# Kernel optimization log

Hardware: AMD Instinct MI355X
Metric: run time of the kernel (lower is better)

The kernel has to match this reference:

```python
import jax, jax.numpy as jnp
import numpy as np

N_NODES = 1_000_000
N_EDGES = 16_000_000
N_IN, HID, N_OUT = 128, 32, 16


def setup_inputs() -> dict:
    key = jax.random.key(0)
    ks = jax.random.split(key, 8)
    x = jax.random.normal(ks[0], (N_NODES, N_IN), dtype=jnp.float32)
    edge_index = jax.random.randint(ks[1], (2, N_EDGES), 0, N_NODES, dtype=jnp.int64)
    edge_weight = jax.random.uniform(ks[2], (N_EDGES,), dtype=jnp.float32)
    # ChebConv(K=1) parameters: one linear per layer + bias
    def glorot(k, fan_in, fan_out):
        s = jnp.sqrt(6.0 / (fan_in + fan_out))
        return jax.random.uniform(k, (fan_in, fan_out), minval=-s, maxval=s, dtype=jnp.float32)
    W0 = glorot(ks[3], N_IN, HID)
    b0 = jnp.zeros((HID,), dtype=jnp.float32)
    W1 = glorot(ks[4], HID, HID)
    b1 = jnp.zeros((HID,), dtype=jnp.float32)
    W2 = glorot(ks[5], HID, N_OUT)
    b2 = jnp.zeros((N_OUT,), dtype=jnp.float32)
    return {"x": x, "edge_index": edge_index, "edge_weight": edge_weight,
            "W0": W0, "b0": b0, "W1": W1, "b1": b1, "W2": W2, "b2": b2}


def reference(x, edge_index, edge_weight, W0, b0, W1, b1, W2, b2):
    # PyG ChebConv with K=1: out = lins[0](Tx_0) + bias, Tx_0 = x.
    # The Laplacian propagation over edge_index/edge_weight is only used for K>=2,
    # so edge_index/edge_weight do not enter the math (kept for signature fidelity).
    h = jax.nn.relu(x @ W0 + b0)      # ChebConv1 + relu
    h = jax.nn.relu(h @ W1 + b1)      # ChebConv2 + relu
    # Dropout(p=0.0) is identity
    return h @ W2 + b2                # ChebConv3 -> [N, nOutputs]
```

## Files before the change

kernel.cpp:

```cpp
#include <hip/hip_runtime.h>


#define N_IN  128
#define HID   32
#define N_OUT 16

using f32x4  = __attribute__((ext_vector_type(4))) float;
using short8 = __attribute__((ext_vector_type(8))) short;
using uint4v = __attribute__((ext_vector_type(4))) unsigned int;

#define N_CHUNKS 22
#define TOTAL_WF_SHORTS (N_CHUNKS * 512)
#define WLDS_GRANULES (N_CHUNKS * 64)

__device__ __forceinline__ unsigned fu(float f) {
    union { float f; unsigned u; } v; v.f = f; return v.u;
}
__device__ __forceinline__ float uf(unsigned u) {
    union { unsigned u; float f; } v; v.u = u; return v.f;
}
__device__ __forceinline__ unsigned short f2bf_rne(float f) {
    unsigned u = fu(f);
    return (unsigned short)((u + 0x7fffu + ((u >> 16) & 1u)) >> 16);
}

__global__ void split_weights(const float* __restrict__ W0,
                              const float* __restrict__ W1,
                              const float* __restrict__ W2,
                              unsigned short* __restrict__ wf) {
    int idx = blockIdx.x * blockDim.x + threadIdx.x;
    if (idx >= TOTAL_WF_SHORTS) return;
    int chunk  = idx >> 9;
    int within = idx & 511;
    int lane = within >> 3;
    int j    = within & 7;
    const float* W; int ncol, k, col, hl;
    if (chunk < 16) {
        int kc = chunk >> 2, nh = (chunk >> 1) & 1; hl = chunk & 1;
        k = kc * 32 + 8 * (lane >> 4) + j; col = nh * 16 + (lane & 15);
        W = W0; ncol = HID;
    } else if (chunk < 20) {
        int c2 = chunk - 16, nh = c2 >> 1; hl = c2 & 1;
        k = 8 * (lane >> 4) + j; col = nh * 16 + (lane & 15);
        W = W1; ncol = HID;
    } else {
        hl = chunk - 20;
        k = 8 * (lane >> 4) + j; col = lane & 15;
        W = W2; ncol = N_OUT;
    }
    float v = W[k * ncol + col];
    unsigned hi_bits = fu(v) & 0xFFFF0000u;
    wf[idx] = (hl == 0) ? (unsigned short)(hi_bits >> 16)
                        : f2bf_rne(v - uf(hi_bits));
}

#define MFMA3(acc, ah, al, bh, bl)                                          \
    do {                                                                    \
        acc = __builtin_amdgcn_mfma_f32_16x16x32_bf16(ah, bh, acc, 0, 0, 0);\
        acc = __builtin_amdgcn_mfma_f32_16x16x32_bf16(al, bh, acc, 0, 0, 0);\
        acc = __builtin_amdgcn_mfma_f32_16x16x32_bf16(ah, bl, acc, 0, 0, 0);\
    } while (0)

__global__ __launch_bounds__(256, 4) void gnn_mfma(
    const float* __restrict__ x, const unsigned short* __restrict__ wf,
    const float* __restrict__ b0, const float* __restrict__ b1,
    const float* __restrict__ b2, float* __restrict__ out,
    int n_tiles, int n_waves_total)
{
    __shared__ __align__(16) unsigned short wlds[N_CHUNKS * 512];
    __shared__ __align__(16) unsigned short hbuf[4][2][16][40];

    const int tid  = threadIdx.x;
    const int wave = tid >> 6;
    const int l    = tid & 63;
    const int r16  = l & 15;
    const int g    = l >> 4;

    {
        const uint4v* wfv = reinterpret_cast<const uint4v*>(wf);
        uint4v* wl = reinterpret_cast<uint4v*>(wlds);
        for (int gg = tid; gg < WLDS_GRANULES; gg += 256)
            wl[gg] = wfv[gg];
    }
    __syncthreads();

    const short8* WL = reinterpret_cast<const short8*>(wlds);

    const float bc0a = b0[r16], bc0b = b0[16 + r16];
    const float bc1a = b1[r16], bc1b = b1[16 + r16];
    const float bc2  = b2[r16];

    const int gw = blockIdx.x * 4 + wave;

    for (int tile = gw; tile < n_tiles; tile += n_waves_total) {
        const int nb = tile * 16;

        f32x4 acc0 = {0.f, 0.f, 0.f, 0.f};
        f32x4 acc1 = {0.f, 0.f, 0.f, 0.f};
        const float* xrow = x + (size_t)(nb + r16) * N_IN + g * 8;

        #pragma unroll
        for (int kc = 0; kc < 4; ++kc) {
            float4 xa = *reinterpret_cast<const float4*>(xrow + kc * 32);
            float4 xb = *reinterpret_cast<const float4*>(xrow + kc * 32 + 4);
            float f[8] = {xa.x, xa.y, xa.z, xa.w, xb.x, xb.y, xb.z, xb.w};
            uint4v hv, lv;
            #pragma unroll
            for (int p = 0; p < 4; ++p) {
                unsigned u0 = fu(f[2 * p]), u1 = fu(f[2 * p + 1]);
                unsigned h0b = u0 & 0xFFFF0000u, h1b = u1 & 0xFFFF0000u;
                hv[p] = h1b | (u0 >> 16);
                float l0 = f[2 * p] - uf(h0b), l1 = f[2 * p + 1] - uf(h1b);
                lv[p] = (fu(l1) & 0xFFFF0000u) | (fu(l0) >> 16);
            }
            short8 ah = __builtin_bit_cast(short8, hv);
            short8 al = __builtin_bit_cast(short8, lv);
            short8 w0h0 = WL[(kc * 4 + 0) * 64 + l];
            short8 w0l0 = WL[(kc * 4 + 1) * 64 + l];
            short8 w0h1 = WL[(kc * 4 + 2) * 64 + l];
            short8 w0l1 = WL[(kc * 4 + 3) * 64 + l];
            MFMA3(acc0, ah, al, w0h0, w0l0);
            MFMA3(acc1, ah, al, w0h1, w0l1);
        }

        #pragma unroll
        for (int i = 0; i < 4; ++i) {
            int row = 4 * g + i;
            float h = fmaxf(acc0[i] + bc0a, 0.f);
            unsigned hb = fu(h) & 0xFFFF0000u;
            hbuf[wave][0][row][r16] = (unsigned short)(hb >> 16);
            hbuf[wave][1][row][r16] = (unsigned short)(fu(h - uf(hb)) >> 16);
            float h2 = fmaxf(acc1[i] + bc0b, 0.f);
            unsigned hb2 = fu(h2) & 0xFFFF0000u;
            hbuf[wave][0][row][16 + r16] = (unsigned short)(hb2 >> 16);
            hbuf[wave][1][row][16 + r16] = (unsigned short)(fu(h2 - uf(hb2)) >> 16);
        }
        short8 h0h = *reinterpret_cast<const short8*>(&hbuf[wave][0][r16][g * 8]);
        short8 h0l = *reinterpret_cast<const short8*>(&hbuf[wave][1][r16][g * 8]);

        f32x4 acc2 = {0.f, 0.f, 0.f, 0.f};
        f32x4 acc3 = {0.f, 0.f, 0.f, 0.f};
        {
            short8 w1h0 = WL[(16 + 0) * 64 + l];
            short8 w1l0 = WL[(16 + 1) * 64 + l];
            short8 w1h1 = WL[(16 + 2) * 64 + l];
            short8 w1l1 = WL[(16 + 3) * 64 + l];
            MFMA3(acc2, h0h, h0l, w1h0, w1l0);
            MFMA3(acc3, h0h, h0l, w1h1, w1l1);
        }
        #pragma unroll
        for (int i = 0; i < 4; ++i) {
            int row = 4 * g + i;
            float h = fmaxf(acc2[i] + bc1a, 0.f);
            unsigned hb = fu(h) & 0xFFFF0000u;
            hbuf[wave][0][row][r16] = (unsigned short)(hb >> 16);
            hbuf[wave][1][row][r16] = (unsigned short)(fu(h - uf(hb)) >> 16);
            float h2 = fmaxf(acc3[i] + bc1b, 0.f);
            unsigned hb2 = fu(h2) & 0xFFFF0000u;
            hbuf[wave][0][row][16 + r16] = (unsigned short)(hb2 >> 16);
            hbuf[wave][1][row][16 + r16] = (unsigned short)(fu(h2 - uf(hb2)) >> 16);
        }
        short8 h1h = *reinterpret_cast<const short8*>(&hbuf[wave][0][r16][g * 8]);
        short8 h1l = *reinterpret_cast<const short8*>(&hbuf[wave][1][r16][g * 8]);

        f32x4 accO = {0.f, 0.f, 0.f, 0.f};
        {
            short8 w2h = WL[(20) * 64 + l];
            short8 w2l = WL[(21) * 64 + l];
            MFMA3(accO, h1h, h1l, w2h, w2l);
        }
        #pragma unroll
        for (int i = 0; i < 4; ++i) {
            int row = 4 * g + i;
            out[(size_t)(nb + row) * N_OUT + r16] = accO[i] + bc2;
        }
    }
}

extern "C" void kernel_launch(void* const* d_in, const int* in_sizes, int n_in,
                              void* d_out, int out_size, void* d_ws, size_t ws_size,
                              hipStream_t stream) {
    const float* x  = (const float*)d_in[0];
    const float* W0 = (const float*)d_in[3];
    const float* b0 = (const float*)d_in[4];
    const float* W1 = (const float*)d_in[5];
    const float* b1 = (const float*)d_in[6];
    const float* W2 = (const float*)d_in[7];
    const float* b2 = (const float*)d_in[8];
    float* out = (float*)d_out;
    unsigned short* wf = (unsigned short*)d_ws;

    int n_nodes = in_sizes[0] / N_IN;
    int n_tiles = n_nodes / 16;

    split_weights<<<(TOTAL_WF_SHORTS + 255) / 256, 256, 0, stream>>>(W0, W1, W2, wf);

    const int n_blocks = 1024;
    const int n_waves_total = n_blocks * 4;
    gnn_mfma<<<dim3(n_blocks), dim3(256), 0, stream>>>(
        x, wf, b0, b1, b2, out, n_tiles, n_waves_total);
}
```

Before: 118.4 us.

## Fuse weight split into main kernel, prefetch next x tile, vectorize output stores

Removes the separate split_weights launch: each block now converts W0/W1/W2 into hi/lo bf16 fragments directly into LDS, which drops one kernel launch but repeats the conversion in every block. The main loop register-double-buffers the next tile's x rows so global loads overlap with the MFMA work on the current tile. Output goes through a small LDS staging buffer so each lane writes a full float4 row segment instead of scattered scalar stores. The extra registers for the prefetch buffer may lower occupancy.

```diff
diff --git a/kernel.cpp b/kernel.cpp
--- a/kernel.cpp
+++ b/kernel.cpp
@@ -10,8 +10,6 @@
 using uint4v = __attribute__((ext_vector_type(4))) unsigned int;
 
 #define N_CHUNKS 22
-#define TOTAL_WF_SHORTS (N_CHUNKS * 512)
-#define WLDS_GRANULES (N_CHUNKS * 64)
 
 __device__ __forceinline__ unsigned fu(float f) {
     union { float f; unsigned u; } v; v.f = f; return v.u;
@@ -22,36 +20,6 @@
 __device__ __forceinline__ unsigned short f2bf_rne(float f) {
     unsigned u = fu(f);
     return (unsigned short)((u + 0x7fffu + ((u >> 16) & 1u)) >> 16);
-}
-
-__global__ void split_weights(const float* __restrict__ W0,
-                              const float* __restrict__ W1,
-                              const float* __restrict__ W2,
-                              unsigned short* __restrict__ wf) {
-    int idx = blockIdx.x * blockDim.x + threadIdx.x;
-    if (idx >= TOTAL_WF_SHORTS) return;
-    int chunk  = idx >> 9;
-    int within = idx & 511;
-    int lane = within >> 3;
-    int j    = within & 7;
-    const float* W; int ncol, k, col, hl;
-    if (chunk < 16) {
-        int kc = chunk >> 2, nh = (chunk >> 1) & 1; hl = chunk & 1;
-        k = kc * 32 + 8 * (lane >> 4) + j; col = nh * 16 + (lane & 15);
-        W = W0; ncol = HID;
-    } else if (chunk < 20) {
-        int c2 = chunk - 16, nh = c2 >> 1; hl = c2 & 1;
-        k = 8 * (lane >> 4) + j; col = nh * 16 + (lane & 15);
-        W = W1; ncol = HID;
-    } else {
-        hl = chunk - 20;
-        k = 8 * (lane >> 4) + j; col = lane & 15;
-        W = W2; ncol = N_OUT;
-    }
-    float v = W[k * ncol + col];
-    unsigned hi_bits = fu(v) & 0xFFFF0000u;
-    wf[idx] = (hl == 0) ? (unsigned short)(hi_bits >> 16)
-                        : f2bf_rne(v - uf(hi_bits));
 }
 
 #define MFMA3(acc, ah, al, bh, bl)                                          \
@@ -62,13 +30,15 @@
     } while (0)
 
 __global__ __launch_bounds__(256, 4) void gnn_mfma(
-    const float* __restrict__ x, const unsigned short* __restrict__ wf,
-    const float* __restrict__ b0, const float* __restrict__ b1,
-    const float* __restrict__ b2, float* __restrict__ out,
-    int n_tiles, int n_waves_total)
+    const float* __restrict__ x,
+    const float* __restrict__ W0, const float* __restrict__ b0,
+    const float* __restrict__ W1, const float* __restrict__ b1,
+    const float* __restrict__ W2, const float* __restrict__ b2,
+    float* __restrict__ out, int n_tiles, int stride)
 {
     __shared__ __align__(16) unsigned short wlds[N_CHUNKS * 512];
     __shared__ __align__(16) unsigned short hbuf[4][2][16][40];
+    __shared__ __align__(16) float sbuf[4][16][20];
 
     const int tid  = threadIdx.x;
     const int wave = tid >> 6;
@@ -76,11 +46,28 @@
     const int r16  = l & 15;
     const int g    = l >> 4;
 
-    {
-        const uint4v* wfv = reinterpret_cast<const uint4v*>(wf);
-        uint4v* wl = reinterpret_cast<uint4v*>(wlds);
-        for (int gg = tid; gg < WLDS_GRANULES; gg += 256)
-            wl[gg] = wfv[gg];
+    for (int c = wave; c < N_CHUNKS; c += 4) {
+        const float* W; int ncol, kbase, col, hl;
+        if (c < 16) {
+            int kc = c >> 2, nh = (c >> 1) & 1; hl = c & 1;
+            W = W0; ncol = HID; kbase = kc * 32 + 8 * (l >> 4); col = nh * 16 + (l & 15);
+        } else if (c < 20) {
+            int c2 = c - 16, nh = c2 >> 1; hl = c2 & 1;
+            W = W1; ncol = HID; kbase = 8 * (l >> 4); col = nh * 16 + (l & 15);
+        } else {
+            hl = c - 20;
+            W = W2; ncol = N_OUT; kbase = 8 * (l >> 4); col = l & 15;
+        }
+        unsigned short tmp[8];
+        #pragma unroll
+        for (int j = 0; j < 8; ++j) {
+            float v = W[(kbase + j) * ncol + col];
+            unsigned hb = fu(v) & 0xFFFF0000u;
+            tmp[j] = (hl == 0) ? (unsigned short)(hb >> 16)
+                               : f2bf_rne(v - uf(hb));
+        }
+        *reinterpret_cast<short8*>(&wlds[c * 512 + l * 8]) =
+            *reinterpret_cast<const short8*>(tmp);
     }
     __syncthreads();
 
@@ -91,18 +78,40 @@
     const float bc2  = b2[r16];
 
     const int gw = blockIdx.x * 4 + wave;
-
-    for (int tile = gw; tile < n_tiles; tile += n_waves_total) {
+    if (gw >= n_tiles) return;
+
+    float4 cur[8];
+    {
+        const float* xr = x + (size_t)(gw * 16 + r16) * N_IN + g * 8;
+        #pragma unroll
+        for (int kc = 0; kc < 4; ++kc) {
+            cur[2 * kc]     = *reinterpret_cast<const float4*>(xr + kc * 32);
+            cur[2 * kc + 1] = *reinterpret_cast<const float4*>(xr + kc * 32 + 4);
+        }
+    }
+
+    for (int tile = gw; tile < n_tiles; tile += stride) {
+        int nt = tile + stride;
+        int pft = (nt < n_tiles) ? nt : tile;
+        float4 nxt[8];
+        {
+            const float* xr = x + (size_t)(pft * 16 + r16) * N_IN + g * 8;
+            #pragma unroll
+            for (int kc = 0; kc < 4; ++kc) {
+                nxt[2 * kc]     = *reinterpret_cast<const float4*>(xr + kc * 32);
+                nxt[2 * kc + 1] = *reinterpret_cast<const float4*>(xr + kc * 32 + 4);
+            }
+        }
+
         const int nb = tile * 16;
 
         f32x4 acc0 = {0.f, 0.f, 0.f, 0.f};
         f32x4 acc1 = {0.f, 0.f, 0.f, 0.f};
-        const float* xrow = x + (size_t)(nb + r16) * N_IN + g * 8;
 
         #pragma unroll
         for (int kc = 0; kc < 4; ++kc) {
-            float4 xa = *reinterpret_cast<const float4*>(xrow + kc * 32);
-            float4 xb = *reinterpret_cast<const float4*>(xrow + kc * 32 + 4);
+            float4 xa = cur[2 * kc];
+            float4 xb = cur[2 * kc + 1];
             float f[8] = {xa.x, xa.y, xa.z, xa.w, xb.x, xb.y, xb.z, xb.w};
             uint4v hv, lv;
             #pragma unroll
@@ -169,11 +178,15 @@
             short8 w2l = WL[(21) * 64 + l];
             MFMA3(accO, h1h, h1l, w2h, w2l);
         }
-        #pragma unroll
-        for (int i = 0; i < 4; ++i) {
-            int row = 4 * g + i;
-            out[(size_t)(nb + row) * N_OUT + r16] = accO[i] + bc2;
-        }
+
+        #pragma unroll
+        for (int i = 0; i < 4; ++i)
+            sbuf[wave][4 * g + i][r16] = accO[i] + bc2;
+        f32x4 ov = *reinterpret_cast<const f32x4*>(&sbuf[wave][l >> 2][(l & 3) * 4]);
+        *reinterpret_cast<f32x4*>(out + (size_t)(nb + (l >> 2)) * N_OUT + (l & 3) * 4) = ov;
+
+        #pragma unroll
+        for (int q = 0; q < 8; ++q) cur[q] = nxt[q];
     }
 }
 
@@ -188,15 +201,12 @@
     const float* W2 = (const float*)d_in[7];
     const float* b2 = (const float*)d_in[8];
     float* out = (float*)d_out;
-    unsigned short* wf = (unsigned short*)d_ws;
 
     int n_nodes = in_sizes[0] / N_IN;
     int n_tiles = n_nodes / 16;
-
-    split_weights<<<(TOTAL_WF_SHORTS + 255) / 256, 256, 0, stream>>>(W0, W1, W2, wf);
 
     const int n_blocks = 1024;
     const int n_waves_total = n_blocks * 4;
     gnn_mfma<<<dim3(n_blocks), dim3(256), 0, stream>>>(
-        x, wf, b0, b1, b2, out, n_tiles, n_waves_total);
-}
+        x, W0, b0, W1, b1, W2, b2, out, n_tiles, n_waves_total);
+}
```

Result: slower. 167.6 us (+41.5%).
